# Optimization experiments

Hardware: AMD Instinct MI355X
Metric: run time of the kernel (lower is better)

## Reference

```python
import jax, jax.numpy as jnp
import numpy as np
import math

B, S, H = 8, 160, 768
DEP = 64
NH, DH = 12, H // 12
W_EDGE = 1.0
EPS = 1e-5


def setup_inputs() -> dict:
    key = jax.random.key(0)
    ks = jax.random.split(key, 16)
    sc_h = 1.0 / math.sqrt(H)
    sc_d = 1.0 / math.sqrt(DEP)
    return {
        "token_feature": jax.random.normal(ks[0], (B, S, H), jnp.float32),
        "edge_feature": jax.random.normal(ks[1], (B, S, S, DEP), jnp.float32),
        "dependency_masks": jax.random.randint(ks[2], (B, S, S), 0, 2, jnp.int32),
        "Wq": jax.random.normal(ks[3], (H, H), jnp.float32) * sc_h,
        "bq": jnp.zeros((H,), jnp.float32),
        "Wk": jax.random.normal(ks[4], (H, H), jnp.float32) * sc_h,
        "bk": jnp.zeros((H,), jnp.float32),
        "Wv": jax.random.normal(ks[5], (H, H), jnp.float32) * sc_h,
        "bv": jnp.zeros((H,), jnp.float32),
        "Wek": jax.random.normal(ks[6], (DEP, H), jnp.float32) * sc_d,
        "bek": jnp.zeros((H,), jnp.float32),
        "Wev": jax.random.normal(ks[7], (DEP, H), jnp.float32) * sc_d,
        "bev": jnp.zeros((H,), jnp.float32),
        "ln_g": jnp.ones((H,), jnp.float32),
        "ln_b": jnp.zeros((H,), jnp.float32),
    }


def _heads3(x):  # [B,S,H] -> [B,NH,S,DH]
    return x.reshape(B, S, NH, DH).transpose(0, 2, 1, 3)


def _heads4(x):  # [B,S,S,H] -> [B,NH,S,S,DH]
    return x.reshape(B, S, S, NH, DH).transpose(0, 3, 1, 2, 4)


def reference(token_feature, edge_feature, dependency_masks,
              Wq, bq, Wk, bk, Wv, bv, Wek, bek, Wev, bev, ln_g, ln_b):
    q = _heads3(token_feature @ Wq + bq)   # [B,NH,S,DH]
    k = _heads3(token_feature @ Wk + bk)
    v = _heads3(token_feature @ Wv + bv)
    ek = _heads4(edge_feature @ Wek + bek)  # [B,NH,S,S,DH]
    ev = _heads4(edge_feature @ Wev + bev)
    # key_ij = k_j + w*ek_ij ; scores_ij = q_i . key_ij / sqrt(dh)
    scores = (jnp.einsum('bhid,bhjd->bhij', q, k)
              + W_EDGE * jnp.einsum('bhid,bhijd->bhij', q, ek))
    scores = scores / math.sqrt(DH)
    mask = (dependency_masks[:, None, :, :] == 0)  # [B,1,S,S]
    scores = jnp.where(mask, jnp.float32(-10000.0), scores)
    probs = jax.nn.softmax(scores, axis=-1)  # dropout is identity in eval
    ctx = (jnp.einsum('bhij,bhjd->bhid', probs, v)
           + W_EDGE * jnp.einsum('bhij,bhijd->bhid', probs, ev))
    ctx = ctx.transpose(0, 2, 1, 3).reshape(B, S, H)
    x = token_feature + ctx
    mu = jnp.mean(x, axis=-1, keepdims=True)
    var = jnp.mean(jnp.square(x - mu), axis=-1, keepdims=True)
    return (x - mu) / jnp.sqrt(var + EPS) * ln_g + ln_b
```

## Files before the change

kernel.cpp:

```cpp
#include <hip/hip_runtime.h>
#include <hip/hip_bf16.h>
#include <math.h>

#define BB 8
#define SS 160
#define HH 768
#define DEPTH 64
#define NHEAD 12
#define DHEAD 64
#define BS (BB*SS)

constexpr float EPS_C = 1e-5f;

typedef __attribute__((ext_vector_type(8))) short bf16x8;
typedef __attribute__((ext_vector_type(4))) float f32x4;

__device__ inline short f2bs(float x) {
    union { __hip_bfloat16 b; short s; } u;
    u.b = __float2bfloat16(x);
    return u.s;
}
__device__ inline float bs2f(short s) {
    union { short s; __hip_bfloat16 b; } u;
    u.s = s;
    return __bfloat162float(u.b);
}

__global__ __launch_bounds__(256) void cast_x(
    const float* __restrict__ X, __hip_bfloat16* __restrict__ Xb)
{
    int idx = blockIdx.x * 256 + threadIdx.x;
    float4 xin = ((const float4*)X)[idx];
    __hip_bfloat16* o = Xb + (size_t)idx * 4;
    o[0] = __float2bfloat16(xin.x); o[1] = __float2bfloat16(xin.y);
    o[2] = __float2bfloat16(xin.z); o[3] = __float2bfloat16(xin.w);
}

__global__ __launch_bounds__(256) void transpose_cast_w(
    const float* __restrict__ Wq, const float* __restrict__ Wk,
    const float* __restrict__ Wv, __hip_bfloat16* __restrict__ WT)
{
    __shared__ float t[32][33];
    const float* W = (blockIdx.z == 0) ? Wq : (blockIdx.z == 1) ? Wk : Wv;
    __hip_bfloat16* o = WT + (size_t)blockIdx.z * HH * HH;
    int kt = blockIdx.x * 32, nt = blockIdx.y * 32;
    int tx = threadIdx.x & 31, ty = threadIdx.x >> 5;
#pragma unroll
    for (int r = 0; r < 32; r += 8)
        t[ty + r][tx] = W[(size_t)(kt + ty + r) * HH + nt + tx];
    __syncthreads();
#pragma unroll
    for (int r = 0; r < 32; r += 8)
        o[(size_t)(nt + ty + r) * HH + kt + tx] = __float2bfloat16(t[tx][ty + r]);
}

__global__ __launch_bounds__(256) void gemm_qkv(
    const __hip_bfloat16* __restrict__ Xb, const __hip_bfloat16* __restrict__ WT,
    const float* __restrict__ bq, const float* __restrict__ bk,
    const float* __restrict__ bv,
    __hip_bfloat16* __restrict__ qb, __hip_bfloat16* __restrict__ kb,
    __hip_bfloat16* __restrict__ vb)
{
    __shared__ int4 sA[4][128];
    __shared__ int4 sB[4][64];
    int m0 = blockIdx.x * 128, n0 = blockIdx.y * 64, mat = blockIdx.z;
    const short* X = (const short*)Xb;
    const short* W = (const short*)WT + (size_t)mat * HH * HH;
    const float* bias = (mat == 0) ? bq : (mat == 1) ? bk : bv;
    int tid = threadIdx.x, w = tid >> 6, l = tid & 63;
    int wm = (w >> 1) * 64, wn = (w & 1) * 32;
    int khalf = l >> 4, lc = l & 15;

    f32x4 acc[4][2];
#pragma unroll
    for (int i = 0; i < 4; i++)
#pragma unroll
        for (int j = 0; j < 2; j++) acc[i][j] = (f32x4){0.f, 0.f, 0.f, 0.f};

    for (int k0 = 0; k0 < HH; k0 += 32) {
        __syncthreads();
        sA[w][l]      = *(const int4*)(X + (size_t)(m0 + l) * HH + k0 + w * 8);
        sA[w][l + 64] = *(const int4*)(X + (size_t)(m0 + l + 64) * HH + k0 + w * 8);
        sB[w][l]      = *(const int4*)(W + (size_t)(n0 + l) * HH + k0 + w * 8);
        __syncthreads();
        bf16x8 b0 = *(const bf16x8*)&sB[khalf][wn + lc];
        bf16x8 b1 = *(const bf16x8*)&sB[khalf][wn + 16 + lc];
#pragma unroll
        for (int mi = 0; mi < 4; mi++) {
            bf16x8 a = *(const bf16x8*)&sA[khalf][wm + mi * 16 + lc];
            acc[mi][0] = __builtin_amdgcn_mfma_f32_16x16x32_bf16(a, b0, acc[mi][0], 0, 0, 0);
            acc[mi][1] = __builtin_amdgcn_mfma_f32_16x16x32_bf16(a, b1, acc[mi][1], 0, 0, 0);
        }
    }

    int rg = (l >> 4) * 4;
    __hip_bfloat16* outm = (mat == 0) ? qb : (mat == 1) ? kb : vb;
#pragma unroll
    for (int ni = 0; ni < 2; ni++) {
        int gcol = n0 + wn + ni * 16 + lc;
        float bv_ = bias[gcol];
#pragma unroll
        for (int mi = 0; mi < 4; mi++) {
            int grow = m0 + wm + mi * 16 + rg;
            f32x4 a = acc[mi][ni];
            __hip_bfloat16* o = outm + (size_t)grow * HH + gcol;
            o[0]      = __float2bfloat16(a.x + bv_);
            o[HH]     = __float2bfloat16(a.y + bv_);
            o[2 * HH] = __float2bfloat16(a.z + bv_);
            o[3 * HH] = __float2bfloat16(a.w + bv_);
        }
    }
}

__global__ __launch_bounds__(256) void scores_gemm(
    const __hip_bfloat16* __restrict__ qb, const __hip_bfloat16* __restrict__ kb,
    _Float16* __restrict__ sc)
{
    __shared__ int4 sQ[8][160];
    __shared__ int4 sK[8][160];
    int h = blockIdx.x, b = blockIdx.y;
    const short* Q = (const short*)qb + (size_t)b * SS * HH + h * DHEAD;
    const short* K = (const short*)kb + (size_t)b * SS * HH + h * DHEAD;
    int tid = threadIdx.x, w = tid >> 6, l = tid & 63;

    for (int idx = tid; idx < SS * 8; idx += 256) {
        int row = idx >> 3, ch = idx & 7;
        sQ[ch][row] = *(const int4*)(Q + (size_t)row * HH + ch * 8);
        sK[ch][row] = *(const int4*)(K + (size_t)row * HH + ch * 8);
    }
    __syncthreads();

    int wm = (w >> 1) * 80, wn = (w & 1) * 80;
    int khalf = l >> 4, lc = l & 15;
    f32x4 acc[5][5];
#pragma unroll
    for (int i = 0; i < 5; i++)
#pragma unroll
        for (int j = 0; j < 5; j++) acc[i][j] = (f32x4){0.f, 0.f, 0.f, 0.f};

#pragma unroll
    for (int s = 0; s < 2; s++) {
        int c = s * 4 + khalf;
        bf16x8 bf[5];
#pragma unroll
        for (int ni = 0; ni < 5; ni++)
            bf[ni] = *(const bf16x8*)&sK[c][wn + ni * 16 + lc];
#pragma unroll
        for (int mi = 0; mi < 5; mi++) {
            bf16x8 a = *(const bf16x8*)&sQ[c][wm + mi * 16 + lc];
#pragma unroll
            for (int ni = 0; ni < 5; ni++)
                acc[mi][ni] = __builtin_amdgcn_mfma_f32_16x16x32_bf16(a, bf[ni], acc[mi][ni], 0, 0, 0);
        }
    }

    int rg = (l >> 4) * 4;
    _Float16* base = sc + (size_t)(b * NHEAD + h) * SS * SS;
#pragma unroll
    for (int mi = 0; mi < 5; mi++) {
        int i0 = wm + mi * 16 + rg;
#pragma unroll
        for (int ni = 0; ni < 5; ni++) {
            int j = wn + ni * 16 + lc;
            f32x4 a = acc[mi][ni];
            base[(size_t)(i0 + 0) * SS + j] = (_Float16)(a.x * 0.125f);
            base[(size_t)(i0 + 1) * SS + j] = (_Float16)(a.y * 0.125f);
            base[(size_t)(i0 + 2) * SS + j] = (_Float16)(a.z * 0.125f);
            base[(size_t)(i0 + 3) * SS + j] = (_Float16)(a.w * 0.125f);
        }
    }
}

__global__ __launch_bounds__(256) void qek_slim(
    const __hip_bfloat16* __restrict__ qb, const float* __restrict__ Wek,
    __hip_bfloat16* __restrict__ qek)
{
    __shared__ short sW[8 * 65 * 8];
    int h = blockIdx.x, mg = blockIdx.y;
    int tid = threadIdx.x, w = tid >> 6, l = tid & 63;
    int lr = l & 15, kg = l >> 4;

    {
        int d = tid >> 2, q4 = tid & 3;
        const float* wp = Wek + (size_t)d * HH + h * DHEAD + q4 * 16;
        float4 w0 = *(const float4*)(wp);
        float4 w1 = *(const float4*)(wp + 4);
        float4 w2 = *(const float4*)(wp + 8);
        float4 w3 = *(const float4*)(wp + 12);
        bf16x8 p0, p1;
        p0[0]=f2bs(w0.x); p0[1]=f2bs(w0.y); p0[2]=f2bs(w0.z); p0[3]=f2bs(w0.w);
        p0[4]=f2bs(w1.x); p0[5]=f2bs(w1.y); p0[6]=f2bs(w1.z); p0[7]=f2bs(w1.w);
        p1[0]=f2bs(w2.x); p1[1]=f2bs(w2.y); p1[2]=f2bs(w2.z); p1[3]=f2bs(w2.w);
        p1[4]=f2bs(w3.x); p1[5]=f2bs(w3.y); p1[6]=f2bs(w3.z); p1[7]=f2bs(w3.w);
        *(bf16x8*)&sW[((q4 * 2) * 65 + d) * 8]     = p0;
        *(bf16x8*)&sW[((q4 * 2 + 1) * 65 + d) * 8] = p1;
    }
    __syncthreads();

    bf16x8 bfrag[2][4];
#pragma unroll
    for (int s = 0; s < 2; s++)
#pragma unroll
        for (int nt = 0; nt < 4; nt++)
            bfrag[s][nt] = *(const bf16x8*)&sW[((s * 4 + kg) * 65 + nt * 16 + lr) * 8];

    const short* Q = (const short*)qb;
    short* O = (short*)qek;
#pragma unroll
    for (int mi = 0; mi < 2; mi++) {
        int m0 = (mg * 8 + w * 2 + mi) * 16;
        bf16x8 a0 = *(const bf16x8*)(Q + (size_t)(m0 + lr) * HH + h * DHEAD + kg * 8);
        bf16x8 a1 = *(const bf16x8*)(Q + (size_t)(m0 + lr) * HH + h * DHEAD + 32 + kg * 8);
#pragma unroll
        for (int nt = 0; nt < 4; nt++) {
            f32x4 acc = (f32x4){0.f, 0.f, 0.f, 0.f};
            acc = __builtin_amdgcn_mfma_f32_16x16x32_bf16(a0, bfrag[0][nt], acc, 0, 0, 0);
            acc = __builtin_amdgcn_mfma_f32_16x16x32_bf16(a1, bfrag[1][nt], acc, 0, 0, 0);
            int row0 = m0 + kg * 4;
#pragma unroll
            for (int r = 0; r < 4; r++)
                O[(size_t)(row0 + r) * HH + h * DHEAD + nt * 16 + lr] = f2bs(acc[r]);
        }
    }
}

__global__ __launch_bounds__(256) void attn_kernel(
    const float* __restrict__ token, const float* __restrict__ edge,
    const int* __restrict__ mask,
    const __hip_bfloat16* __restrict__ q_ws, const _Float16* __restrict__ sc,
    const __hip_bfloat16* __restrict__ v_ws, const __hip_bfloat16* __restrict__ qek,
    const float* __restrict__ bek,
    const float* __restrict__ Wev, const float* __restrict__ bev,
    const float* __restrict__ ln_g, const float* __restrict__ ln_b,
    float* __restrict__ out)
{
    __shared__ float  s_ctx[HH];
    __shared__ float  s_scores[NHEAD][SS];
    __shared__ float  s_pe[NHEAD][DEPTH];
    __shared__ float  s_x[HH];
    __shared__ float  s_qbek[NHEAD];
    __shared__ int    s_mask[SS];
    __shared__ float  s_red[8];

    int bi = blockIdx.x;
    int b  = bi / SS;
    int i  = bi - b * SS;
    int tid = threadIdx.x;
    int w = tid >> 6, l = tid & 63;
    int lr = l & 15, kg = l >> 4;

    if (tid < SS) s_mask[tid] = mask[(size_t)bi * SS + tid];

    {
        int hs = w * 3 + kg;
        float part = 0.f;
        if (hs < NHEAD) {
            const __hip_bfloat16* qp = q_ws + (size_t)bi * HH + hs * DHEAD + lr * 4;
            float4 bv4 = *(const float4*)(bek + hs * DHEAD + lr * 4);
            part = __bfloat162float(qp[0]) * bv4.x + __bfloat162float(qp[1]) * bv4.y
                 + __bfloat162float(qp[2]) * bv4.z + __bfloat162float(qp[3]) * bv4.w;
        }
        part += __shfl_xor(part, 1, 64);
        part += __shfl_xor(part, 2, 64);
        part += __shfl_xor(part, 4, 64);
        part += __shfl_xor(part, 8, 64);
        if (lr == 0 && hs < NHEAD) s_qbek[hs] = part;
    }
    __syncthreads();

    const _Float16* scp = sc + (size_t)(b * NHEAD) * (SS * SS) + (size_t)i * SS;
    for (int idx = tid; idx < NHEAD * SS; idx += 256) {
        int h = idx / SS, j = idx - h * SS;
        float qk = (float)scp[(size_t)h * (SS * SS) + j];
        s_scores[h][j] = s_mask[j] ? (qk + 0.125f * s_qbek[h]) : -10000.0f;
    }
    __syncthreads();

    const float* e_row = edge + (size_t)bi * SS * DEPTH;
    {
        const short* QE = (const short*)qek + (size_t)bi * HH;
        bf16x8 qe0 = *(const bf16x8*)(QE + lr * DHEAD + kg * 8);
        bf16x8 qe1 = *(const bf16x8*)(QE + lr * DHEAD + 32 + kg * 8);
        for (int jt = w; jt < 10; jt += 4) {
            const float* ep = e_row + (size_t)(jt * 16 + lr) * DEPTH + kg * 8;
            float4 e0 = *(const float4*)(ep);
            float4 e1 = *(const float4*)(ep + 4);
            float4 e2 = *(const float4*)(ep + 32);
            float4 e3 = *(const float4*)(ep + 36);
            bf16x8 a0, a1;
            a0[0]=f2bs(e0.x); a0[1]=f2bs(e0.y); a0[2]=f2bs(e0.z); a0[3]=f2bs(e0.w);
            a0[4]=f2bs(e1.x); a0[5]=f2bs(e1.y); a0[6]=f2bs(e1.z); a0[7]=f2bs(e1.w);
            a1[0]=f2bs(e2.x); a1[1]=f2bs(e2.y); a1[2]=f2bs(e2.z); a1[3]=f2bs(e2.w);
            a1[4]=f2bs(e3.x); a1[5]=f2bs(e3.y); a1[6]=f2bs(e3.z); a1[7]=f2bs(e3.w);
            f32x4 acc = (f32x4){0.f, 0.f, 0.f, 0.f};
            acc = __builtin_amdgcn_mfma_f32_16x16x32_bf16(a0, qe0, acc, 0, 0, 0);
            acc = __builtin_amdgcn_mfma_f32_16x16x32_bf16(a1, qe1, acc, 0, 0, 0);
            if (lr < NHEAD) {
                int j0 = jt * 16 + kg * 4;
#pragma unroll
                for (int r = 0; r < 4; r++)
                    if (s_mask[j0 + r])
                        s_scores[lr][j0 + r] += 0.125f * acc[r];
            }
        }
    }
    __syncthreads();

    for (int h = w; h < NHEAD; h += 4) {
        float v0 = s_scores[h][l];
        float v1 = s_scores[h][l + 64];
        float v2 = (l < 32) ? s_scores[h][l + 128] : -INFINITY;
        float mx = fmaxf(v0, fmaxf(v1, v2));
#pragma unroll
        for (int mm = 32; mm >= 1; mm >>= 1) mx = fmaxf(mx, __shfl_xor(mx, mm, 64));
        float e0 = expf(v0 - mx), e1 = expf(v1 - mx);
        float e2 = (l < 32) ? expf(v2 - mx) : 0.f;
        float sm = e0 + e1 + e2;
#pragma unroll
        for (int mm = 32; mm >= 1; mm >>= 1) sm += __shfl_xor(sm, mm, 64);
        float inv = 1.0f / sm;
        s_scores[h][l]      = e0 * inv;
        s_scores[h][l + 64] = e1 * inv;
        if (l < 32) s_scores[h][l + 128] = e2 * inv;
    }
    __syncthreads();

    {
        int h0 = w * 3;
        float av0 = 0.f, av1 = 0.f, av2 = 0.f;
        float pe0 = 0.f, pe1 = 0.f, pe2 = 0.f;
        const __hip_bfloat16* vbp = v_ws + (size_t)b * SS * HH + h0 * DHEAD + l;
        const float* er = e_row + l;
#pragma unroll 2
        for (int j0 = 0; j0 < SS; j0 += 2) {
            float2 p0 = *(const float2*)(&s_scores[h0][j0]);
            float2 p1 = *(const float2*)(&s_scores[h0 + 1][j0]);
            float2 p2 = *(const float2*)(&s_scores[h0 + 2][j0]);
            const __hip_bfloat16* vp = vbp + (size_t)j0 * HH;
            av0 += p0.x * __bfloat162float(vp[0])
                 + p0.y * __bfloat162float(vp[HH]);
            av1 += p1.x * __bfloat162float(vp[DHEAD])
                 + p1.y * __bfloat162float(vp[HH + DHEAD]);
            av2 += p2.x * __bfloat162float(vp[2 * DHEAD])
                 + p2.y * __bfloat162float(vp[HH + 2 * DHEAD]);
            float ev0 = er[(size_t)j0 * DEPTH];
            float ev1 = er[(size_t)(j0 + 1) * DEPTH];
            pe0 += p0.x * ev0 + p0.y * ev1;
            pe1 += p1.x * ev0 + p1.y * ev1;
            pe2 += p2.x * ev0 + p2.y * ev1;
        }
        s_pe[h0][l]     = pe0;
        s_pe[h0 + 1][l] = pe1;
        s_pe[h0 + 2][l] = pe2;
        s_ctx[h0 * DHEAD + l]       = av0;
        s_ctx[(h0 + 1) * DHEAD + l] = av1;
        s_ctx[(h0 + 2) * DHEAD + l] = av2;
    }
    __syncthreads();

    for (int mdx = tid; mdx < HH; mdx += 256) {
        int h = mdx >> 6;
        const float* pep = &s_pe[h][0];
        float sum = 0.f;
#pragma unroll
        for (int d = 0; d < DEPTH; d++) sum += pep[d] * Wev[(size_t)d * HH + mdx];
        float ctx = s_ctx[mdx] + (sum + bev[mdx]);
        s_x[mdx] = token[(size_t)bi * HH + mdx] + ctx;
    }
    __syncthreads();

    float lsum = 0.f, lsq = 0.f;
    for (int c = tid; c < HH; c += 256) {
        float x = s_x[c];
        lsum += x; lsq += x * x;
    }
#pragma unroll
    for (int mm = 32; mm >= 1; mm >>= 1) {
        lsum += __shfl_xor(lsum, mm, 64);
        lsq  += __shfl_xor(lsq,  mm, 64);
    }
    if (l == 0) { s_red[w] = lsum; s_red[4 + w] = lsq; }
    __syncthreads();
    float tsum = s_red[0] + s_red[1] + s_red[2] + s_red[3];
    float tsq  = s_red[4] + s_red[5] + s_red[6] + s_red[7];
    float mu  = tsum / HH;
    float var = tsq / HH - mu * mu;
    float rstd = rsqrtf(var + EPS_C);
    for (int c = tid; c < HH; c += 256)
        out[(size_t)bi * HH + c] = (s_x[c] - mu) * rstd * ln_g[c] + ln_b[c];
}

extern "C" void kernel_launch(void* const* d_in, const int* in_sizes, int n_in,
                              void* d_out, int out_size, void* d_ws, size_t ws_size,
                              hipStream_t stream) {
    const float* token = (const float*)d_in[0];
    const float* edge  = (const float*)d_in[1];
    const int*   mask  = (const int*)d_in[2];
    const float* Wq = (const float*)d_in[3];  const float* bq = (const float*)d_in[4];
    const float* Wk = (const float*)d_in[5];  const float* bk = (const float*)d_in[6];
    const float* Wv = (const float*)d_in[7];  const float* bv = (const float*)d_in[8];
    const float* Wek = (const float*)d_in[9];  const float* bek = (const float*)d_in[10];
    const float* Wev = (const float*)d_in[11]; const float* bev = (const float*)d_in[12];
    const float* ln_g = (const float*)d_in[13]; const float* ln_b = (const float*)d_in[14];
    float* out = (float*)d_out;

    __hip_bfloat16* qb = (__hip_bfloat16*)d_ws;
    __hip_bfloat16* kb = qb + (size_t)BS * HH;
    __hip_bfloat16* vb = kb + (size_t)BS * HH;
    __hip_bfloat16* Xb = vb + (size_t)BS * HH;
    __hip_bfloat16* WT = Xb + (size_t)BS * HH;
    _Float16*       sc = (_Float16*)Xb;
    __hip_bfloat16* qek = kb;

    cast_x<<<(BS * HH / 4) / 256, 256, 0, stream>>>(token, Xb);
    transpose_cast_w<<<dim3(24, 24, 3), 256, 0, stream>>>(Wq, Wk, Wv, WT);
    gemm_qkv<<<dim3(BS / 128, HH / 64, 3), 256, 0, stream>>>(
        Xb, WT, bq, bk, bv, qb, kb, vb);
    scores_gemm<<<dim3(NHEAD, BB), 256, 0, stream>>>(qb, kb, sc);
    qek_slim<<<dim3(NHEAD, 10), 256, 0, stream>>>(qb, Wek, qek);
    attn_kernel<<<BS, 256, 0, stream>>>(token, edge, mask, qb, sc, vb, qek,
                                        bek, Wev, bev, ln_g, ln_b, out);
}
```

Baseline: 111.3 us.

## Fuse token cast into QKV GEMM and relayout scores for row-contiguous reads

Drops the separate cast_x kernel: gemm_qkv now loads fp32 token rows and converts them to bf16 while staging into shared memory. The scores buffer is relaid out as [b,i,h,j] so each attention block reads one contiguous row pair-wise as packed halves, and s_scores is padded. qek_slim uses twice as many blocks with one m-tile per wave. This removes a launch and a round trip through the bf16 copy of X, but the GEMM now reads fp32 X once per N-tile (12 column blocks × 3 matrices), and the scores writes become strided. sc reuses the WT region, which is still read by gemm_qkv; this is safe only because kernels on the stream run in order.

```diff
diff --git a/kernel.cpp b/kernel.cpp
--- a/kernel.cpp
+++ b/kernel.cpp
@@ -9,6 +9,7 @@
 #define NHEAD 12
 #define DHEAD 64
 #define BS (BB*SS)
+#define SCROW (NHEAD*SS)
 
 constexpr float EPS_C = 1e-5f;
 
@@ -19,21 +20,6 @@
     union { __hip_bfloat16 b; short s; } u;
     u.b = __float2bfloat16(x);
     return u.s;
-}
-__device__ inline float bs2f(short s) {
-    union { short s; __hip_bfloat16 b; } u;
-    u.s = s;
-    return __bfloat162float(u.b);
-}
-
-__global__ __launch_bounds__(256) void cast_x(
-    const float* __restrict__ X, __hip_bfloat16* __restrict__ Xb)
-{
-    int idx = blockIdx.x * 256 + threadIdx.x;
-    float4 xin = ((const float4*)X)[idx];
-    __hip_bfloat16* o = Xb + (size_t)idx * 4;
-    o[0] = __float2bfloat16(xin.x); o[1] = __float2bfloat16(xin.y);
-    o[2] = __float2bfloat16(xin.z); o[3] = __float2bfloat16(xin.w);
 }
 
 __global__ __launch_bounds__(256) void transpose_cast_w(
@@ -55,7 +41,7 @@
 }
 
 __global__ __launch_bounds__(256) void gemm_qkv(
-    const __hip_bfloat16* __restrict__ Xb, const __hip_bfloat16* __restrict__ WT,
+    const float* __restrict__ X, const __hip_bfloat16* __restrict__ WT,
     const float* __restrict__ bq, const float* __restrict__ bk,
     const float* __restrict__ bv,
     __hip_bfloat16* __restrict__ qb, __hip_bfloat16* __restrict__ kb,
@@ -64,7 +50,6 @@
     __shared__ int4 sA[4][128];
     __shared__ int4 sB[4][64];
     int m0 = blockIdx.x * 128, n0 = blockIdx.y * 64, mat = blockIdx.z;
-    const short* X = (const short*)Xb;
     const short* W = (const short*)WT + (size_t)mat * HH * HH;
     const float* bias = (mat == 0) ? bq : (mat == 1) ? bk : bv;
     int tid = threadIdx.x, w = tid >> 6, l = tid & 63;
@@ -79,9 +64,17 @@
 
     for (int k0 = 0; k0 < HH; k0 += 32) {
         __syncthreads();
-        sA[w][l]      = *(const int4*)(X + (size_t)(m0 + l) * HH + k0 + w * 8);
-        sA[w][l + 64] = *(const int4*)(X + (size_t)(m0 + l + 64) * HH + k0 + w * 8);
-        sB[w][l]      = *(const int4*)(W + (size_t)(n0 + l) * HH + k0 + w * 8);
+#pragma unroll
+        for (int rr = 0; rr < 2; rr++) {
+            const float* ap = X + (size_t)(m0 + l + rr * 64) * HH + k0 + w * 8;
+            float4 x0 = *(const float4*)ap;
+            float4 x1 = *(const float4*)(ap + 4);
+            bf16x8 p;
+            p[0]=f2bs(x0.x); p[1]=f2bs(x0.y); p[2]=f2bs(x0.z); p[3]=f2bs(x0.w);
+            p[4]=f2bs(x1.x); p[5]=f2bs(x1.y); p[6]=f2bs(x1.z); p[7]=f2bs(x1.w);
+            *(bf16x8*)&sA[w][l + rr * 64] = p;
+        }
+        sB[w][l] = *(const int4*)(W + (size_t)(n0 + l) * HH + k0 + w * 8);
         __syncthreads();
         bf16x8 b0 = *(const bf16x8*)&sB[khalf][wn + lc];
         bf16x8 b1 = *(const bf16x8*)&sB[khalf][wn + 16 + lc];
@@ -155,7 +148,7 @@
     }
 
     int rg = (l >> 4) * 4;
-    _Float16* base = sc + (size_t)(b * NHEAD + h) * SS * SS;
+    _Float16* base = sc + ((size_t)b * SS) * SCROW + (size_t)h * SS;
 #pragma unroll
     for (int mi = 0; mi < 5; mi++) {
         int i0 = wm + mi * 16 + rg;
@@ -163,10 +156,10 @@
         for (int ni = 0; ni < 5; ni++) {
             int j = wn + ni * 16 + lc;
             f32x4 a = acc[mi][ni];
-            base[(size_t)(i0 + 0) * SS + j] = (_Float16)(a.x * 0.125f);
-            base[(size_t)(i0 + 1) * SS + j] = (_Float16)(a.y * 0.125f);
-            base[(size_t)(i0 + 2) * SS + j] = (_Float16)(a.z * 0.125f);
-            base[(size_t)(i0 + 3) * SS + j] = (_Float16)(a.w * 0.125f);
+            base[(size_t)(i0 + 0) * SCROW + j] = (_Float16)(a.x * 0.125f);
+            base[(size_t)(i0 + 1) * SCROW + j] = (_Float16)(a.y * 0.125f);
+            base[(size_t)(i0 + 2) * SCROW + j] = (_Float16)(a.z * 0.125f);
+            base[(size_t)(i0 + 3) * SCROW + j] = (_Float16)(a.w * 0.125f);
         }
     }
 }
@@ -206,21 +199,18 @@
 
     const short* Q = (const short*)qb;
     short* O = (short*)qek;
-#pragma unroll
-    for (int mi = 0; mi < 2; mi++) {
-        int m0 = (mg * 8 + w * 2 + mi) * 16;
-        bf16x8 a0 = *(const bf16x8*)(Q + (size_t)(m0 + lr) * HH + h * DHEAD + kg * 8);
-        bf16x8 a1 = *(const bf16x8*)(Q + (size_t)(m0 + lr) * HH + h * DHEAD + 32 + kg * 8);
-#pragma unroll
-        for (int nt = 0; nt < 4; nt++) {
-            f32x4 acc = (f32x4){0.f, 0.f, 0.f, 0.f};
-            acc = __builtin_amdgcn_mfma_f32_16x16x32_bf16(a0, bfrag[0][nt], acc, 0, 0, 0);
-            acc = __builtin_amdgcn_mfma_f32_16x16x32_bf16(a1, bfrag[1][nt], acc, 0, 0, 0);
-            int row0 = m0 + kg * 4;
-#pragma unroll
-            for (int r = 0; r < 4; r++)
-                O[(size_t)(row0 + r) * HH + h * DHEAD + nt * 16 + lr] = f2bs(acc[r]);
-        }
+    int m0 = (mg * 4 + w) * 16;
+    bf16x8 a0 = *(const bf16x8*)(Q + (size_t)(m0 + lr) * HH + h * DHEAD + kg * 8);
+    bf16x8 a1 = *(const bf16x8*)(Q + (size_t)(m0 + lr) * HH + h * DHEAD + 32 + kg * 8);
+#pragma unroll
+    for (int nt = 0; nt < 4; nt++) {
+        f32x4 acc = (f32x4){0.f, 0.f, 0.f, 0.f};
+        acc = __builtin_amdgcn_mfma_f32_16x16x32_bf16(a0, bfrag[0][nt], acc, 0, 0, 0);
+        acc = __builtin_amdgcn_mfma_f32_16x16x32_bf16(a1, bfrag[1][nt], acc, 0, 0, 0);
+        int row0 = m0 + kg * 4;
+#pragma unroll
+        for (int r = 0; r < 4; r++)
+            O[(size_t)(row0 + r) * HH + h * DHEAD + nt * 16 + lr] = f2bs(acc[r]);
     }
 }
 
@@ -235,7 +225,7 @@
     float* __restrict__ out)
 {
     __shared__ float  s_ctx[HH];
-    __shared__ float  s_scores[NHEAD][SS];
+    __shared__ float  s_scores[NHEAD][SS + 2];
     __shared__ float  s_pe[NHEAD][DEPTH];
     __shared__ float  s_x[HH];
     __shared__ float  s_qbek[NHEAD];
@@ -244,7 +234,6 @@
 
     int bi = blockIdx.x;
     int b  = bi / SS;
-    int i  = bi - b * SS;
     int tid = threadIdx.x;
     int w = tid >> 6, l = tid & 63;
     int lr = l & 15, kg = l >> 4;
@@ -268,11 +257,14 @@
     }
     __syncthreads();
 
-    const _Float16* scp = sc + (size_t)(b * NHEAD) * (SS * SS) + (size_t)i * SS;
-    for (int idx = tid; idx < NHEAD * SS; idx += 256) {
-        int h = idx / SS, j = idx - h * SS;
-        float qk = (float)scp[(size_t)h * (SS * SS) + j];
-        s_scores[h][j] = s_mask[j] ? (qk + 0.125f * s_qbek[h]) : -10000.0f;
+    const float* scf = (const float*)(sc + (size_t)bi * SCROW);
+    for (int idx = tid; idx < SCROW / 2; idx += 256) {
+        int h = idx / (SS / 2), jp = idx - h * (SS / 2);
+        union { float f; _Float16 e[2]; } u;
+        u.f = scf[idx];
+        int j = jp * 2;
+        s_scores[h][j]     = s_mask[j]     ? ((float)u.e[0] + 0.125f * s_qbek[h]) : -10000.0f;
+        s_scores[h][j + 1] = s_mask[j + 1] ? ((float)u.e[1] + 0.125f * s_qbek[h]) : -10000.0f;
     }
     __syncthreads();
 
@@ -407,17 +399,15 @@
     __hip_bfloat16* qb = (__hip_bfloat16*)d_ws;
     __hip_bfloat16* kb = qb + (size_t)BS * HH;
     __hip_bfloat16* vb = kb + (size_t)BS * HH;
-    __hip_bfloat16* Xb = vb + (size_t)BS * HH;
-    __hip_bfloat16* WT = Xb + (size_t)BS * HH;
-    _Float16*       sc = (_Float16*)Xb;
+    __hip_bfloat16* WT = vb + (size_t)BS * HH;
+    _Float16*       sc = (_Float16*)WT;
     __hip_bfloat16* qek = kb;
 
-    cast_x<<<(BS * HH / 4) / 256, 256, 0, stream>>>(token, Xb);
     transpose_cast_w<<<dim3(24, 24, 3), 256, 0, stream>>>(Wq, Wk, Wv, WT);
     gemm_qkv<<<dim3(BS / 128, HH / 64, 3), 256, 0, stream>>>(
-        Xb, WT, bq, bk, bv, qb, kb, vb);
+        token, WT, bq, bk, bv, qb, kb, vb);
     scores_gemm<<<dim3(NHEAD, BB), 256, 0, stream>>>(qb, kb, sc);
-    qek_slim<<<dim3(NHEAD, 10), 256, 0, stream>>>(qb, Wek, qek);
+    qek_slim<<<dim3(NHEAD, 20), 256, 0, stream>>>(qb, Wek, qek);
     attn_kernel<<<BS, 256, 0, stream>>>(token, edge, mask, qb, sc, vb, qek,
                                         bek, Wev, bev, ln_g, ln_b, out);
 }
```

Measured after the change: 113.1 us. No clear change (+1.6%).
